# Kernel tuning notes

Measured on AMD Instinct MI355X. Metric: run time of the kernel, lower is better.

Reference implementation:

```python
import jax, jax.numpy as jnp
import numpy as np

N, E, G = 50000, 400000, 64
IN_C, HID, OUT_C, HEADS = 256, 128, 256, 4
LRELU_SLOPE = 0.2
LN_EPS = 1e-5


def setup_inputs() -> dict:
    key = jax.random.key(0)
    ks = jax.random.split(key, 16)
    d = {}
    d["x"] = jax.random.normal(ks[0], (N, IN_C), dtype=jnp.float32)
    d["edge_index"] = jax.random.randint(ks[1], (2, E), 0, N, dtype=jnp.int32)
    d["batch"] = jnp.sort(jax.random.randint(ks[2], (N,), 0, G, dtype=jnp.int32))
    s1 = 1.0 / np.sqrt(IN_C)
    d["W1"] = jax.random.uniform(ks[3], (IN_C, HEADS * HID), jnp.float32, -s1, s1)
    d["att_src1"] = jax.random.normal(ks[4], (HEADS, HID), jnp.float32) * 0.1
    d["att_dst1"] = jax.random.normal(ks[5], (HEADS, HID), jnp.float32) * 0.1
    d["b1"] = jnp.zeros((HEADS * HID,), jnp.float32)
    d["ln1_g"] = jnp.ones((HEADS * HID,), jnp.float32)
    d["ln1_b"] = jnp.zeros((HEADS * HID,), jnp.float32)
    s2 = 1.0 / np.sqrt(HEADS * HID)
    d["W2"] = jax.random.uniform(ks[6], (HEADS * HID, OUT_C), jnp.float32, -s2, s2)
    d["att_src2"] = jax.random.normal(ks[7], (1, OUT_C), jnp.float32) * 0.1
    d["att_dst2"] = jax.random.normal(ks[8], (1, OUT_C), jnp.float32) * 0.1
    d["b2"] = jnp.zeros((OUT_C,), jnp.float32)
    d["ln2_g"] = jnp.ones((OUT_C,), jnp.float32)
    d["ln2_b"] = jnp.zeros((OUT_C,), jnp.float32)
    return d


def _layernorm(x, g, b):
    mu = jnp.mean(x, axis=-1, keepdims=True)
    var = jnp.mean(jnp.square(x - mu), axis=-1, keepdims=True)
    return (x - mu) * jax.lax.rsqrt(var + LN_EPS) * g + b


def _gat_conv(x, src, dst, W, a_src, a_dst, bias):
    # PyG GATConv (eval mode, dropout inactive), self-loops already in src/dst.
    H, C = a_src.shape
    h = (x @ W).reshape(N, H, C)                       # [N,H,C]
    e_src = jnp.einsum('nhc,hc->nh', h, a_src)          # [N,H]
    e_dst = jnp.einsum('nhc,hc->nh', h, a_dst)
    e = jax.nn.leaky_relu(e_src[src] + e_dst[dst], LRELU_SLOPE)  # [Etot,H]
    m = jax.ops.segment_max(e, dst, num_segments=N)     # segment softmax over incoming edges
    ex = jnp.exp(e - m[dst])
    s = jax.ops.segment_sum(ex, dst, num_segments=N)
    alpha = ex / (s[dst] + 1e-16)                       # [Etot,H]
    msg = h[src] * alpha[:, :, None]                    # [Etot,H,C]
    out = jax.ops.segment_sum(msg, dst, num_segments=N) # [N,H,C]
    return out.reshape(N, H * C) + bias


def reference(x, edge_index, batch, W1, att_src1, att_dst1, b1, ln1_g, ln1_b,
              W2, att_src2, att_dst2, b2, ln2_g, ln2_b):
    loops = jnp.arange(N, dtype=edge_index.dtype)
    src = jnp.concatenate([edge_index[0], loops])
    dst = jnp.concatenate([edge_index[1], loops])
    h = _gat_conv(x, src, dst, W1, att_src1, att_dst1, b1)
    h = _layernorm(h, ln1_g, ln1_b)
    h = jax.nn.relu(h)                                  # dropout is identity in eval
    h = _gat_conv(h, src, dst, W2, att_src2, att_dst2, b2)
    h = _layernorm(h, ln2_g, ln2_b)
    # global_mean_pool over graphs
    sums = jax.ops.segment_sum(h, batch, num_segments=G)
    cnts = jax.ops.segment_sum(jnp.ones((N,), h.dtype), batch, num_segments=G)
    return sums / jnp.maximum(cnts, 1.0)[:, None]
```

## Files before the change

kernel.cpp:

```cpp
#include <hip/hip_runtime.h>
#include <hip/hip_bf16.h>
#include <cstdint>

#define LRELU_SLOPE 0.2f

typedef short bf16x8 __attribute__((ext_vector_type(8)));
typedef float f32x4  __attribute__((ext_vector_type(4)));

__device__ __forceinline__ float b2f(unsigned short u) {
  return __uint_as_float(((unsigned int)u) << 16);
}
__device__ __forceinline__ unsigned short f2b(float f) {
  unsigned int u = __float_as_uint(f);
  return (unsigned short)((u + 0x7fff + ((u >> 16) & 1)) >> 16);
}

__device__ __forceinline__ void gload16(const void* g, void* l) {
  __builtin_amdgcn_global_load_lds(
      (const __attribute__((address_space(1))) unsigned int*)g,
      (__attribute__((address_space(3))) unsigned int*)l, 16, 0, 0);
}

__global__ __launch_bounds__(256)
void prep_x_count(const float* __restrict__ x, unsigned short* __restrict__ o,
                  int M, int Mpad, const int* __restrict__ ei, int E, int Etot,
                  int* __restrict__ count) {
  const int i = blockIdx.x * 256 + threadIdx.x;
  if (i < Mpad * 64) {
    const int row = i >> 6;
    const int c4  = (i & 63) * 4;
    ushort4 v = make_ushort4(0, 0, 0, 0);
    if (row < M) {
      const float4 f = *(const float4*)&x[(size_t)row * 256 + c4];
      v = make_ushort4(f2b(f.x), f2b(f.y), f2b(f.z), f2b(f.w));
    }
    *(ushort4*)&o[(size_t)row * 256 + c4] = v;
  }
  if (i < Etot) {
    const int d = (i < E) ? ei[E + i] : (i - E);
    atomicAdd(&count[d], 1);
  }
}

__global__ __launch_bounds__(256)
void cvt_wts(const float* __restrict__ W1, const float* __restrict__ W2,
             unsigned short* __restrict__ W1T, unsigned short* __restrict__ W2T) {
  int j = blockIdx.x * 256 + threadIdx.x;
  if (j < 512 * 256) {
    const int n = j >> 8, k = j & 255;
    W1T[j] = f2b(W1[(size_t)k * 512 + n]);
  } else {
    j -= 512 * 256;
    const int n = j >> 9, k = j & 511;
    W2T[j] = f2b(W2[(size_t)k * 256 + n]);
  }
}

__global__ __launch_bounds__(256)
void scan_blocksum(const int* __restrict__ count, int* __restrict__ bsum, int Nn) {
  const int i0 = blockIdx.x * 1024 + threadIdx.x * 4;
  int s = 0;
#pragma unroll
  for (int k = 0; k < 4; ++k) { const int i = i0 + k; if (i < Nn) s += count[i]; }
#pragma unroll
  for (int off = 1; off < 64; off <<= 1) s += __shfl_xor(s, off);
  __shared__ int ws[4];
  if ((threadIdx.x & 63) == 0) ws[threadIdx.x >> 6] = s;
  __syncthreads();
  if (threadIdx.x == 0) bsum[blockIdx.x] = ws[0] + ws[1] + ws[2] + ws[3];
}

__global__ __launch_bounds__(64)
void scan_top(const int* __restrict__ bsum, int* __restrict__ boff,
              int* __restrict__ rowptrN, int nb) {
  const int t = threadIdx.x;
  const int v = (t < nb) ? bsum[t] : 0;
  int incl = v;
#pragma unroll
  for (int off = 1; off < 64; off <<= 1) {
    const int u = __shfl_up(incl, off);
    if (t >= off) incl += u;
  }
  if (t < nb) boff[t] = incl - v;
  if (t == 63) *rowptrN = incl;
}

__global__ __launch_bounds__(256)
void scan_apply(const int* __restrict__ count, const int* __restrict__ boff,
                int* __restrict__ rowptr, int* __restrict__ cursor, int Nn) {
  const int t = threadIdx.x;
  const int lane = t & 63;
  const int w = t >> 6;
  const int i0 = blockIdx.x * 1024 + t * 4;
  int c[4]; int s = 0;
#pragma unroll
  for (int k = 0; k < 4; ++k) { const int i = i0 + k; c[k] = (i < Nn) ? count[i] : 0; s += c[k]; }
  int incl = s;
#pragma unroll
  for (int off = 1; off < 64; off <<= 1) {
    const int u = __shfl_up(incl, off);
    if (lane >= off) incl += u;
  }
  __shared__ int ws[4];
  if (lane == 63) ws[w] = incl;
  __syncthreads();
  int woff = 0;
  for (int k = 0; k < w; ++k) woff += ws[k];
  int base = boff[blockIdx.x] + woff + incl - s;
#pragma unroll
  for (int k = 0; k < 4; ++k) {
    const int i = i0 + k;
    if (i < Nn) { rowptr[i] = base; cursor[i] = base; base += c[k]; }
  }
}

__global__ __launch_bounds__(256)
void csr_scatter(const int* __restrict__ ei, int E, int Etot,
                 int* __restrict__ cursor, int* __restrict__ srcs,
                 int* __restrict__ dsts) {
  const int i = blockIdx.x * 256 + threadIdx.x;
  if (i >= Etot) return;
  const int s = (i < E) ? ei[i]     : (i - E);
  const int d = (i < E) ? ei[E + i] : (i - E);
  const int pos = atomicAdd(&cursor[d], 1);
  srcs[pos] = s;
  dsts[pos] = d;
}

template<int KSTEPS>
__global__ __launch_bounds__(256)
void gemm_bf16(const unsigned short* __restrict__ A,
               const unsigned short* __restrict__ BT,
               unsigned short* __restrict__ C, int M, int Nn, int K,
               const float* __restrict__ asrc, const float* __restrict__ adst,
               float* __restrict__ es, float* __restrict__ ed,
               int H, int lgC) {
  __shared__ unsigned short As[2][128 * 32];
  __shared__ unsigned short Bs[2][128 * 32];
  const int tid  = threadIdx.x;
  const int lane = tid & 63;
  const int wave = tid >> 6;
  const int wm = wave >> 1, wn = wave & 1;
  const int brow = blockIdx.y * 128;
  const int bcol = blockIdx.x * 128;
  const int srow  = tid >> 2;
  const int sslot = tid & 3;
  const int sswz  = sslot ^ (srow & 3);
  const size_t aBase0 = (size_t)(brow + srow) * K + sswz * 8;
  const size_t aBase1 = (size_t)(brow + 64 + srow) * K + sswz * 8;
  const size_t bBase0 = (size_t)(bcol + srow) * K + sswz * 8;
  const size_t bBase1 = (size_t)(bcol + 64 + srow) * K + sswz * 8;
  const int ldsOff0 = srow * 32 + sslot * 8;
  const int ldsOff1 = (64 + srow) * 32 + sslot * 8;

  f32x4 acc[4][4] = {};
  const int u   = lane >> 4;
  const int r15 = lane & 15;
  const int sw  = u ^ (r15 & 3);

  auto stage = [&](int buf, int ks) {
    const int k0 = ks * 32;
    gload16(A + aBase0 + k0, &As[buf][ldsOff0]);
    gload16(A + aBase1 + k0, &As[buf][ldsOff1]);
    gload16(BT + bBase0 + k0, &Bs[buf][ldsOff0]);
    gload16(BT + bBase1 + k0, &Bs[buf][ldsOff1]);
  };

  stage(0, 0);
  asm volatile("s_waitcnt vmcnt(0)" ::: "memory");
  __syncthreads();
  int cur = 0;
#pragma unroll
  for (int ks = 0; ks < KSTEPS; ++ks) {
    if (ks + 1 < KSTEPS) stage(cur ^ 1, ks + 1);
    bf16x8 af[4], bfv[4];
#pragma unroll
    for (int m = 0; m < 4; ++m) {
      const int row = wm * 64 + m * 16 + r15;
      af[m]  = *(const bf16x8*)&As[cur][row * 32 + sw * 8];
      const int col = wn * 64 + m * 16 + r15;
      bfv[m] = *(const bf16x8*)&Bs[cur][col * 32 + sw * 8];
    }
#pragma unroll
    for (int m = 0; m < 4; ++m)
#pragma unroll
      for (int n = 0; n < 4; ++n)
        acc[m][n] = __builtin_amdgcn_mfma_f32_16x16x32_bf16(
            af[m], bfv[n], acc[m][n], 0, 0, 0);
    if (ks + 1 < KSTEPS) {
      asm volatile("s_waitcnt vmcnt(0)" ::: "memory");
      __syncthreads();
      cur ^= 1;
    }
  }
#pragma unroll
  for (int m = 0; m < 4; ++m) {
    const int r0 = brow + wm * 64 + m * 16 + u * 4;
#pragma unroll
    for (int n = 0; n < 4; ++n) {
      const int cc = bcol + wn * 64 + n * 16 + r15;
#pragma unroll
      for (int r = 0; r < 4; ++r)
        if (r0 + r < M) C[(size_t)(r0 + r) * Nn + cc] = f2b(acc[m][n][r]);
    }
  }
  const int head = bcol >> lgC;
  float asv[4], adv[4];
#pragma unroll
  for (int n = 0; n < 4; ++n) {
    const int cc = bcol + wn * 64 + n * 16 + r15;
    asv[n] = asrc[cc];
    adv[n] = adst[cc];
  }
#pragma unroll
  for (int m = 0; m < 4; ++m) {
#pragma unroll
    for (int r = 0; r < 4; ++r) {
      float pes = 0.f, ped = 0.f;
#pragma unroll
      for (int n = 0; n < 4; ++n) {
        pes = fmaf(acc[m][n][r], asv[n], pes);
        ped = fmaf(acc[m][n][r], adv[n], ped);
      }
#pragma unroll
      for (int off = 1; off < 16; off <<= 1) {
        pes += __shfl_xor(pes, off);
        ped += __shfl_xor(ped, off);
      }
      if (r15 == 0) {
        const int row = brow + wm * 64 + m * 16 + u * 4 + r;
        if (row < M) {
          unsafeAtomicAdd(&es[row * H + head], pes);
          unsafeAtomicAdd(&ed[row * H + head], ped);
        }
      }
    }
  }
}

template<int H>
__global__ __launch_bounds__(256)
void ex_compute(const int* __restrict__ srcs, const int* __restrict__ dsts,
                const float* __restrict__ es, const float* __restrict__ ed,
                float* __restrict__ exCSR, int Etot) {
  const int p = blockIdx.x * 256 + threadIdx.x;
  if (p >= Etot) return;
  const int sN = srcs[p], dN = dsts[p];
  if constexpr (H == 4) {
    const float4 a = *(const float4*)&es[sN * 4];
    const float4 b = *(const float4*)&ed[dN * 4];
    float e0 = a.x + b.x, e1 = a.y + b.y, e2 = a.z + b.z, e3 = a.w + b.w;
    e0 = (e0 > 0.f) ? e0 : LRELU_SLOPE * e0;
    e1 = (e1 > 0.f) ? e1 : LRELU_SLOPE * e1;
    e2 = (e2 > 0.f) ? e2 : LRELU_SLOPE * e2;
    e3 = (e3 > 0.f) ? e3 : LRELU_SLOPE * e3;
    *(float4*)&exCSR[p * 4] =
        make_float4(__expf(e0), __expf(e1), __expf(e2), __expf(e3));
  } else {
    float e = es[sN] + ed[dN];
    e = (e > 0.f) ? e : LRELU_SLOPE * e;
    exCSR[p] = __expf(e);
  }
}

template<int H, int C, bool RELU, bool BFOUT>
__global__ __launch_bounds__(256)
void gat_agg_ln(const int* __restrict__ rowptr, const int* __restrict__ srcs,
                const float* __restrict__ exCSR,
                const unsigned short* __restrict__ h,
                const float* __restrict__ bias, const float* __restrict__ lng,
                const float* __restrict__ lnb, unsigned short* __restrict__ obf,
                float* __restrict__ of32, int Nn) {
  constexpr int HC = H * C;
  constexpr int F  = HC / 64;
  const int wave = threadIdx.x >> 6;
  const int lane = threadIdx.x & 63;
  const int n = blockIdx.x * 4 + wave;
  if (n >= Nn) return;
  const int beg = rowptr[n];
  const int deg = rowptr[n + 1] - beg;
  const int hl = (lane * F) / C;

  float dsum = 0.f;
  if constexpr (H == 4) {
    for (int it = lane; it < deg * 4; it += 64) dsum += exCSR[beg * 4 + it];
#pragma unroll
    for (int off = 4; off < 64; off <<= 1) dsum += __shfl_xor(dsum, off);
    dsum = __shfl(dsum, hl);
  } else {
    for (int it = lane; it < deg; it += 64) dsum += exCSR[beg + it];
#pragma unroll
    for (int off = 1; off < 64; off <<= 1) dsum += __shfl_xor(dsum, off);
  }
  const float inv_s = 1.0f / (dsum + 1e-16f);

  float acc[F];
#pragma unroll
  for (int i = 0; i < F; ++i) acc[i] = 0.f;

  auto fma_rows = [&](const ushort4* v0, const ushort4* v1, const float* a, int cnt) {
    for (int q = 0; q < cnt; ++q) {
      acc[0] = fmaf(b2f(v0[q].x), a[q], acc[0]);
      acc[1] = fmaf(b2f(v0[q].y), a[q], acc[1]);
      acc[2] = fmaf(b2f(v0[q].z), a[q], acc[2]);
      acc[3] = fmaf(b2f(v0[q].w), a[q], acc[3]);
      if constexpr (F == 8) {
        acc[4] = fmaf(b2f(v1[q].x), a[q], acc[4]);
        acc[5] = fmaf(b2f(v1[q].y), a[q], acc[5]);
        acc[6] = fmaf(b2f(v1[q].z), a[q], acc[6]);
        acc[7] = fmaf(b2f(v1[q].w), a[q], acc[7]);
      }
    }
  };

  int j = 0;
  for (; j + 4 <= deg; j += 4) {
    int s4[4];
    float a4[4];
#pragma unroll
    for (int q = 0; q < 4; ++q) s4[q] = srcs[beg + j + q];
#pragma unroll
    for (int q = 0; q < 4; ++q) a4[q] = exCSR[(beg + j + q) * H + hl] * inv_s;
    ushort4 v0[4], v1[4];
#pragma unroll
    for (int q = 0; q < 4; ++q) {
      const unsigned short* hp = &h[(size_t)s4[q] * HC + lane * F];
      v0[q] = *(const ushort4*)hp;
      if constexpr (F == 8) v1[q] = *(const ushort4*)(hp + 4);
    }
    fma_rows(v0, v1, a4, 4);
  }
  for (; j < deg; ++j) {
    const int src = srcs[beg + j];
    const float a = exCSR[(beg + j) * H + hl] * inv_s;
    const unsigned short* hp = &h[(size_t)src * HC + lane * F];
    ushort4 v0 = *(const ushort4*)hp, v1;
    if constexpr (F == 8) v1 = *(const ushort4*)(hp + 4);
    fma_rows(&v0, &v1, &a, 1);
  }

#pragma unroll
  for (int i = 0; i < F; i += 4) {
    const float4 bb = *(const float4*)&bias[lane * F + i];
    acc[i + 0] += bb.x; acc[i + 1] += bb.y;
    acc[i + 2] += bb.z; acc[i + 3] += bb.w;
  }
  float sum = 0.f, sq = 0.f;
#pragma unroll
  for (int i = 0; i < F; ++i) { sum += acc[i]; sq += acc[i] * acc[i]; }
#pragma unroll
  for (int off = 1; off < 64; off <<= 1) {
    sum += __shfl_xor(sum, off);
    sq  += __shfl_xor(sq, off);
  }
  const float mu  = sum / HC;
  const float var = sq / HC - mu * mu;
  const float r   = rsqrtf(var + 1e-5f);
  float y[F];
#pragma unroll
  for (int i = 0; i < F; i += 4) {
    const float4 gg = *(const float4*)&lng[lane * F + i];
    const float4 bl = *(const float4*)&lnb[lane * F + i];
    y[i + 0] = (acc[i + 0] - mu) * r * gg.x + bl.x;
    y[i + 1] = (acc[i + 1] - mu) * r * gg.y + bl.y;
    y[i + 2] = (acc[i + 2] - mu) * r * gg.z + bl.z;
    y[i + 3] = (acc[i + 3] - mu) * r * gg.w + bl.w;
  }
  if constexpr (RELU) {
#pragma unroll
    for (int i = 0; i < F; ++i) y[i] = fmaxf(y[i], 0.f);
  }
  if constexpr (BFOUT) {
    unsigned short* op = &obf[(size_t)n * HC + lane * F];
    *(ushort4*)op = make_ushort4(f2b(y[0]), f2b(y[1]), f2b(y[2]), f2b(y[3]));
    if constexpr (F == 8)
      *(ushort4*)(op + 4) = make_ushort4(f2b(y[4]), f2b(y[5]), f2b(y[6]), f2b(y[7]));
  } else {
    float* op = &of32[(size_t)n * HC + lane * F];
    *(float4*)op = make_float4(y[0], y[1], y[2], y[3]);
    if constexpr (F == 8)
      *(float4*)(op + 4) = make_float4(y[4], y[5], y[6], y[7]);
  }
}

__global__ __launch_bounds__(256)
void pool_partial(const unsigned short* __restrict__ x, const int* __restrict__ batch,
                  float* __restrict__ tmp, int* __restrict__ cnt, int Nn) {
  const int r0 = blockIdx.x * 64;
  const int rend = min(r0 + 64, Nn);
  const int t = threadIdx.x;
  float acc = 0.f;
  int cur = batch[r0];
  int seglen = 0;
  for (int r = r0; r < rend; ++r) {
    const int g = batch[r];
    if (g != cur) {
      unsafeAtomicAdd(&tmp[cur * 256 + t], acc);
      if (t == 0) atomicAdd(&cnt[cur], seglen);
      acc = 0.f; seglen = 0; cur = g;
    }
    acc += b2f(x[(size_t)r * 256 + t]);
    ++seglen;
  }
  unsafeAtomicAdd(&tmp[cur * 256 + t], acc);
  if (t == 0) atomicAdd(&cnt[cur], seglen);
}

__global__ __launch_bounds__(256)
void pool_final(const float* __restrict__ tmp, const int* __restrict__ cnt,
                float* __restrict__ out) {
  const int g = blockIdx.x;
  const int t = threadIdx.x;
  out[g * 256 + t] = tmp[g * 256 + t] / fmaxf((float)cnt[g], 1.f);
}

extern "C" void kernel_launch(void* const* d_in, const int* in_sizes, int n_in,
                              void* d_out, int out_size, void* d_ws, size_t ws_size,
                              hipStream_t stream) {
  const float* x    = (const float*)d_in[0];
  const int*   ei   = (const int*)d_in[1];
  const int*   batch= (const int*)d_in[2];
  const float* W1   = (const float*)d_in[3];
  const float* as1  = (const float*)d_in[4];
  const float* ad1  = (const float*)d_in[5];
  const float* b1   = (const float*)d_in[6];
  const float* g1   = (const float*)d_in[7];
  const float* be1  = (const float*)d_in[8];
  const float* W2   = (const float*)d_in[9];
  const float* as2  = (const float*)d_in[10];
  const float* ad2  = (const float*)d_in[11];
  const float* b2   = (const float*)d_in[12];
  const float* g2   = (const float*)d_in[13];
  const float* be2  = (const float*)d_in[14];

  const int N    = in_sizes[0] / 256;
  const int E    = in_sizes[1] / 2;
  const int Etot = E + N;
  const int Mpad = ((N + 127) / 128) * 128;
  const int NB   = (N + 1023) / 1024;

  float* ws = (float*)d_ws;
  unsigned short* out2 = (unsigned short*)ws;
  unsigned short* A2bf = out2 + (size_t)N * 256;
  unsigned short* A1bf = A2bf;
  unsigned short* h1bf = A2bf + (size_t)Mpad * 512;
  unsigned short* W1T  = h1bf + (size_t)N * 512;
  unsigned short* W2T  = W1T + 512 * 256;
  float* es1 = (float*)(W2T + 512 * 256);
  float* ed1 = es1 + (size_t)N * 4;
  float* es2 = ed1 + (size_t)N * 4;
  float* ed2 = es2 + N;
  int* count  = (int*)(ed2 + N);
  int* rowptr = count + N;
  int* cursor = rowptr + N + 4;
  int* srcs   = cursor + N;
  int* dsts   = srcs + Etot;
  float* exCSR = (float*)(dsts + Etot);
  float* ptmp = exCSR + (size_t)Etot * 4;
  int*   pcnt = (int*)(ptmp + 64 * 256);
  int*   bsum = pcnt + 64;
  int*   boff = bsum + 64;
  unsigned short* h2bf = h1bf;

  const int eb = (Etot + 255) / 256;

  hipMemsetAsync(es1, 0, (size_t)N * 11 * 4, stream);
  hipMemsetAsync(ptmp, 0, (size_t)(64 * 256 + 64) * 4, stream);
  hipMemsetAsync(A2bf + (size_t)N * 512, 0, (size_t)(Mpad - N) * 512 * 2, stream);

  prep_x_count<<<(Mpad * 64 + 255) / 256, 256, 0, stream>>>(
      x, A1bf, N, Mpad, ei, E, Etot, count);
  cvt_wts<<<(2 * 512 * 256 + 255) / 256, 256, 0, stream>>>(W1, W2, W1T, W2T);

  scan_blocksum<<<NB, 256, 0, stream>>>(count, bsum, N);
  scan_top<<<1, 64, 0, stream>>>(bsum, boff, &rowptr[N], NB);
  scan_apply<<<NB, 256, 0, stream>>>(count, boff, rowptr, cursor, N);
  csr_scatter<<<eb, 256, 0, stream>>>(ei, E, Etot, cursor, srcs, dsts);

  gemm_bf16<8><<<dim3(4, Mpad / 128), 256, 0, stream>>>(
      A1bf, W1T, h1bf, N, 512, 256, as1, ad1, es1, ed1, 4, 7);
  ex_compute<4><<<eb, 256, 0, stream>>>(srcs, dsts, es1, ed1, exCSR, Etot);
  gat_agg_ln<4, 128, true, true><<<(N + 3) / 4, 256, 0, stream>>>(
      rowptr, srcs, exCSR, h1bf, b1, g1, be1, A2bf, nullptr, N);

  gemm_bf16<16><<<dim3(2, Mpad / 128), 256, 0, stream>>>(
      A2bf, W2T, h2bf, N, 256, 512, as2, ad2, es2, ed2, 1, 8);
  ex_compute<1><<<eb, 256, 0, stream>>>(srcs, dsts, es2, ed2, exCSR, Etot);
  gat_agg_ln<1, 256, false, true><<<(N + 3) / 4, 256, 0, stream>>>(
      rowptr, srcs, exCSR, h2bf, b2, g2, be2, out2, nullptr, N);

  pool_partial<<<(N + 63) / 64, 256, 0, stream>>>(out2, batch, ptmp, pcnt, N);
  pool_final<<<64, 256, 0, stream>>>(ptmp, pcnt, (float*)d_out);
}
```

Measured before the change: 340.0 us.

## Triple-buffer GEMM loads and split layer-2 attention partials per column block

The GEMM moves from double to triple buffering in LDS. Loads run two k-steps ahead, waits are partial (vmcnt(4)), and there is a single barrier per step, so more global-load latency can overlap the MFMA work. For layer 2, each column block writes its attention-score partials to a separate buffer instead of atomically adding into one slot, which removes atomic contention. ex_compute then sums the two partials. This uses more LDS per block, which may lower occupancy, and needs a larger zeroed workspace.

```diff
diff --git a/kernel.cpp b/kernel.cpp
--- a/kernel.cpp
+++ b/kernel.cpp
@@ -134,9 +134,9 @@
                unsigned short* __restrict__ C, int M, int Nn, int K,
                const float* __restrict__ asrc, const float* __restrict__ adst,
                float* __restrict__ es, float* __restrict__ ed,
-               int H, int lgC) {
-  __shared__ unsigned short As[2][128 * 32];
-  __shared__ unsigned short Bs[2][128 * 32];
+               int H, int lgC, int esPart) {
+  __shared__ unsigned short As[3][128 * 32];
+  __shared__ unsigned short Bs[3][128 * 32];
   const int tid  = threadIdx.x;
   const int lane = tid & 63;
   const int wave = tid >> 6;
@@ -152,6 +152,8 @@
   const size_t bBase1 = (size_t)(bcol + 64 + srow) * K + sswz * 8;
   const int ldsOff0 = srow * 32 + sslot * 8;
   const int ldsOff1 = (64 + srow) * 32 + sslot * 8;
+  es += (size_t)blockIdx.x * esPart;
+  ed += (size_t)blockIdx.x * esPart;
 
   f32x4 acc[4][4] = {};
   const int u   = lane >> 4;
@@ -167,12 +169,16 @@
   };
 
   stage(0, 0);
-  asm volatile("s_waitcnt vmcnt(0)" ::: "memory");
-  __syncthreads();
-  int cur = 0;
+  stage(1, 1);
 #pragma unroll
   for (int ks = 0; ks < KSTEPS; ++ks) {
-    if (ks + 1 < KSTEPS) stage(cur ^ 1, ks + 1);
+    if (ks + 1 < KSTEPS)
+      asm volatile("s_waitcnt vmcnt(4)" ::: "memory");
+    else
+      asm volatile("s_waitcnt vmcnt(0)" ::: "memory");
+    __builtin_amdgcn_s_barrier();
+    if (ks + 2 < KSTEPS) stage((ks + 2) % 3, ks + 2);
+    const int cur = ks % 3;
     bf16x8 af[4], bfv[4];
 #pragma unroll
     for (int m = 0; m < 4; ++m) {
@@ -187,11 +193,6 @@
       for (int n = 0; n < 4; ++n)
         acc[m][n] = __builtin_amdgcn_mfma_f32_16x16x32_bf16(
             af[m], bfv[n], acc[m][n], 0, 0, 0);
-    if (ks + 1 < KSTEPS) {
-      asm volatile("s_waitcnt vmcnt(0)" ::: "memory");
-      __syncthreads();
-      cur ^= 1;
-    }
   }
 #pragma unroll
   for (int m = 0; m < 4; ++m) {
@@ -242,7 +243,7 @@
 __global__ __launch_bounds__(256)
 void ex_compute(const int* __restrict__ srcs, const int* __restrict__ dsts,
                 const float* __restrict__ es, const float* __restrict__ ed,
-                float* __restrict__ exCSR, int Etot) {
+                float* __restrict__ exCSR, int Etot, int pN) {
   const int p = blockIdx.x * 256 + threadIdx.x;
   if (p >= Etot) return;
   const int sN = srcs[p], dN = dsts[p];
@@ -257,7 +258,7 @@
     *(float4*)&exCSR[p * 4] =
         make_float4(__expf(e0), __expf(e1), __expf(e2), __expf(e3));
   } else {
-    float e = es[sN] + ed[dN];
+    float e = (es[sN] + es[pN + sN]) + (ed[dN] + ed[pN + dN]);
     e = (e > 0.f) ? e : LRELU_SLOPE * e;
     exCSR[p] = __expf(e);
   }
@@ -449,8 +450,8 @@
   float* es1 = (float*)(W2T + 512 * 256);
   float* ed1 = es1 + (size_t)N * 4;
   float* es2 = ed1 + (size_t)N * 4;
-  float* ed2 = es2 + N;
-  int* count  = (int*)(ed2 + N);
+  float* ed2 = es2 + (size_t)N * 2;
+  int* count  = (int*)(ed2 + (size_t)N * 2);
   int* rowptr = count + N;
   int* cursor = rowptr + N + 4;
   int* srcs   = cursor + N;
@@ -464,7 +465,7 @@
 
   const int eb = (Etot + 255) / 256;
 
-  hipMemsetAsync(es1, 0, (size_t)N * 11 * 4, stream);
+  hipMemsetAsync(es1, 0, (size_t)N * 13 * 4, stream);
   hipMemsetAsync(ptmp, 0, (size_t)(64 * 256 + 64) * 4, stream);
   hipMemsetAsync(A2bf + (size_t)N * 512, 0, (size_t)(Mpad - N) * 512 * 2, stream);
 
@@ -478,14 +479,14 @@
   csr_scatter<<<eb, 256, 0, stream>>>(ei, E, Etot, cursor, srcs, dsts);
 
   gemm_bf16<8><<<dim3(4, Mpad / 128), 256, 0, stream>>>(
-      A1bf, W1T, h1bf, N, 512, 256, as1, ad1, es1, ed1, 4, 7);
-  ex_compute<4><<<eb, 256, 0, stream>>>(srcs, dsts, es1, ed1, exCSR, Etot);
+      A1bf, W1T, h1bf, N, 512, 256, as1, ad1, es1, ed1, 4, 7, 0);
+  ex_compute<4><<<eb, 256, 0, stream>>>(srcs, dsts, es1, ed1, exCSR, Etot, 0);
   gat_agg_ln<4, 128, true, true><<<(N + 3) / 4, 256, 0, stream>>>(
       rowptr, srcs, exCSR, h1bf, b1, g1, be1, A2bf, nullptr, N);
 
   gemm_bf16<16><<<dim3(2, Mpad / 128), 256, 0, stream>>>(
-      A2bf, W2T, h2bf, N, 256, 512, as2, ad2, es2, ed2, 1, 8);
-  ex_compute<1><<<eb, 256, 0, stream>>>(srcs, dsts, es2, ed2, exCSR, Etot);
+      A2bf, W2T, h2bf, N, 256, 512, as2, ad2, es2, ed2, 1, 8, N);
+  ex_compute<1><<<eb, 256, 0, stream>>>(srcs, dsts, es2, ed2, exCSR, Etot, N);
   gat_agg_ln<1, 256, false, true><<<(N + 3) / 4, 256, 0, stream>>>(
       rowptr, srcs, exCSR, h2bf, b2, g2, be2, out2, nullptr, N);
 
```

New measurement: 333.9 us. About the same (-1.8%).
